# Performance work log

Measured on AMD Instinct MI355X. Metric: run time of the kernel, lower is better.

The kernel has to match this reference:

```python
import jax, jax.numpy as jnp
import numpy as np

N, M, D = 2048, 50000, 128


def setup_inputs() -> dict:
    key = jax.random.key(0)
    kz, kr = jax.random.split(key)
    z = jax.random.normal(kz, (N, D), dtype=jnp.float32)
    ref = jax.random.normal(kr, (M, D), dtype=jnp.float32)  # stands in for the concatenated in_dl batches
    return {"z": z, "ref": ref, "k": 10}


def reference(z, ref, k):
    # L2-normalize rows (matches z / z.norm(dim=1, keepdim=True))
    zn = z / jnp.linalg.norm(z, axis=1, keepdims=True)      # [N, D]
    rn = ref / jnp.linalg.norm(ref, axis=1, keepdims=True)  # [M, D]
    # Pairwise L2 distances via ||a||^2 + ||b||^2 - 2 a.b (same math as the
    # broadcast (rep_batch - rep_z).norm(dim=2), without the O(N*M*D) blowup).
    sq = (jnp.sum(zn * zn, axis=1)[:, None]
          + jnp.sum(rn * rn, axis=1)[None, :]
          - 2.0 * jnp.einsum('nd,md->nm', zn, rn))          # [N, M]
    dist = jnp.sqrt(jnp.maximum(sq, 1e-12))
    # Full sort along the reference axis, take the k-th smallest distance.
    return jnp.sort(dist, axis=1)[:, k]                      # [N]
```

## Files before the change

### kernel.cpp

```cpp
#include <hip/hip_runtime.h>


#define D_DIM 128
#define TQB 256
#define BR 64
#define NCH 64
#define NSUB (NCH * 16)
#define KK 11
#define CAP 256

typedef __bf16 bf16_t;
typedef bf16_t bf16x8 __attribute__((ext_vector_type(8)));
typedef float f32x16 __attribute__((ext_vector_type(16)));

__device__ __forceinline__ unsigned short f2bf(float f) {
    unsigned u = __float_as_uint(f);
    return (unsigned short)((u + 0x7fffu + ((u >> 16) & 1u)) >> 16);
}

__global__ __launch_bounds__(256) void normalize_bf16(
    const float* __restrict__ z, const float* __restrict__ ref,
    unsigned short* __restrict__ zb, unsigned short* __restrict__ rb,
    int N, int M)
{
    const int w = threadIdx.x >> 6;
    const int l = threadIdx.x & 63;
    const int row = blockIdx.x * 4 + w;
    if (row >= N + M) return;
    const float* in; unsigned short* out; int r;
    if (row < N) { in = z;   out = zb; r = row; }
    else         { in = ref; out = rb; r = row - N; }
    const float2 v = ((const float2*)in)[(size_t)r * 64 + l];
    float ss = v.x * v.x + v.y * v.y;
    #pragma unroll
    for (int off = 32; off > 0; off >>= 1) ss += __shfl_xor(ss, off);
    const float inv = rsqrtf(ss);
    ushort2 o; o.x = f2bf(v.x * inv); o.y = f2bf(v.y * inv);
    ((ushort2*)out)[(size_t)r * 64 + l] = o;
}

__device__ __forceinline__ void gld_lds16(const unsigned short* g,
                                          unsigned short* l) {
    __builtin_amdgcn_global_load_lds(
        (__attribute__((address_space(1))) void*)g,
        (__attribute__((address_space(3))) void*)l, 16, 0, 0);
}

template <int PASS>
__global__ __launch_bounds__(512) void knn_pass(
    const unsigned short* __restrict__ zb, const unsigned short* __restrict__ rb,
    float* __restrict__ maxes, const float* __restrict__ T,
    int* __restrict__ cnt, float* __restrict__ surv,
    int N, int M, int chunk)
{
    __shared__ __align__(16) unsigned short Bt[2 * BR * D_DIM];

    const int nwg = 8 * NCH;
    const int bid = (int)blockIdx.x + 8 * (int)blockIdx.y;
    const int swz = (bid & 7) * (nwg >> 3) + (bid >> 3);
    const int bx = swz & 7;
    const int by = swz >> 3;

    const int t = threadIdx.x;
    const int lane = t & 63;
    const int w = t >> 6;
    const int quad = lane >> 4;
    const int ln = lane & 15;
    const int l31 = lane & 31;
    const int hi = lane >> 5;
    const int rbase = bx * TQB + w * 32;
    const int row = rbase + l31;
    const int c0 = by * chunk;
    const int c1 = min(c0 + chunk, M);
    const int clen = c1 - c0;
    const int nt = (clen + BR - 1) / BR;

    bf16x8 qfr[8];
    #pragma unroll
    for (int ks = 0; ks < 8; ++ks)
        qfr[ks] = *(const bf16x8*)
            &zb[(size_t)row * D_DIM + ks * 16 + hi * 8];

    float mx[16];
    float tr = 0.f;
    if (PASS == 1) {
        #pragma unroll
        for (int r = 0; r < 16; ++r) mx[r] = -3.0f;
    } else {
        tr = T[row];
    }

    auto stage = [&](int half, int tile) {
        const int s0 = c0 + tile * BR;
        #pragma unroll
        for (int i = 0; i < 2; ++i) {
            const int r = w * 8 + i * 4 + quad;
            int g = s0 + r; if (g > M - 1) g = M - 1;
            const int sl = ln ^ (r & 15);
            gld_lds16(&rb[(size_t)g * D_DIM + sl * 8],
                      &Bt[half * (BR * D_DIM) + (w * 8 + i * 4) * D_DIM]);
        }
    };

    stage(0, 0);
    stage(1, nt > 1 ? 1 : 0);

    for (int it = 0; it < nt; ++it) {
        if (it + 1 < nt) asm volatile("s_waitcnt vmcnt(2)" ::: "memory");
        else             asm volatile("s_waitcnt vmcnt(0)" ::: "memory");
        __builtin_amdgcn_s_barrier();
        asm volatile("" ::: "memory");
        __builtin_amdgcn_sched_barrier(0);

        const int cur = it & 1;
        const unsigned short* Bc = &Bt[cur * (BR * D_DIM)];

        f32x16 acc0 = {0,0,0,0,0,0,0,0,0,0,0,0,0,0,0,0};
        f32x16 acc1 = {0,0,0,0,0,0,0,0,0,0,0,0,0,0,0,0};

        __builtin_amdgcn_s_setprio(1);
        #pragma unroll
        for (int ks = 0; ks < 8; ++ks) {
            const int sl = ((ks * 2 + hi) ^ ln) * 8;
            bf16x8 a0 = *(const bf16x8*)&Bc[(l31)      * D_DIM + sl];
            bf16x8 a1 = *(const bf16x8*)&Bc[(32 + l31) * D_DIM + sl];
            acc0 = __builtin_amdgcn_mfma_f32_32x32x16_bf16(a0, qfr[ks], acc0, 0, 0, 0);
            acc1 = __builtin_amdgcn_mfma_f32_32x32x16_bf16(a1, qfr[ks], acc1, 0, 0, 0);
        }
        __builtin_amdgcn_s_setprio(0);

        const int rem = clen - it * BR;
        if (rem >= BR) {
            if (PASS == 1) {
                #pragma unroll
                for (int r = 0; r < 16; ++r)
                    mx[r] = fmaxf(mx[r], fmaxf(acc0[r], acc1[r]));
            } else {
                #pragma unroll
                for (int r = 0; r < 16; ++r) {
                    float v0 = acc0[r], v1 = acc1[r];
                    if (v0 >= tr) {
                        int slot = atomicAdd(&cnt[row], 1);
                        if (slot < CAP) surv[(size_t)row * CAP + slot] = v0;
                    }
                    if (v1 >= tr) {
                        int slot = atomicAdd(&cnt[row], 1);
                        if (slot < CAP) surv[(size_t)row * CAP + slot] = v1;
                    }
                }
            }
        } else {
            #pragma unroll
            for (int r = 0; r < 16; ++r) {
                const int crow = (r & 3) + 8 * (r >> 2) + 4 * hi;
                const bool ok0 = crow < rem;
                const bool ok1 = 32 + crow < rem;
                if (PASS == 1) {
                    if (ok0) mx[r] = fmaxf(mx[r], acc0[r]);
                    if (ok1) mx[r] = fmaxf(mx[r], acc1[r]);
                } else {
                    float v0 = acc0[r], v1 = acc1[r];
                    if (ok0 && v0 >= tr) {
                        int slot = atomicAdd(&cnt[row], 1);
                        if (slot < CAP) surv[(size_t)row * CAP + slot] = v0;
                    }
                    if (ok1 && v1 >= tr) {
                        int slot = atomicAdd(&cnt[row], 1);
                        if (slot < CAP) surv[(size_t)row * CAP + slot] = v1;
                    }
                }
            }
        }

        __builtin_amdgcn_sched_barrier(0);
        asm volatile("" ::: "memory");
        __builtin_amdgcn_s_barrier();
        if (it + 2 < nt) stage(cur, it + 2);
    }

    if (PASS == 1) {
        #pragma unroll
        for (int r = 0; r < 16; ++r) {
            float m2 = fmaxf(mx[r], __shfl_xor(mx[r], 32));
            if (hi == 0)
                maxes[(size_t)row * NSUB + by * 16 + r] = m2;
        }
    }
}

__device__ __forceinline__ float kth_largest_64(float* s, int kk, int t) {
    float cur = -3.0f;
    for (int it = 0; it <= kk; ++it) {
        float m = s[0];
        #pragma unroll
        for (int off = 32; off > 0; off >>= 1) m = fmaxf(m, __shfl_xor(m, off));
        cur = m;
        unsigned long long b = __ballot(s[0] == m);
        bool owner = ((int)(__ffsll(b) - 1) == t);
        #pragma unroll
        for (int j = 0; j < KK - 1; ++j) s[j] = owner ? s[j + 1] : s[j];
        if (owner) s[KK - 1] = -3.0f;
    }
    return cur;
}

__global__ __launch_bounds__(64) void knn_threshold(
    const float* __restrict__ maxes, const int* __restrict__ kp,
    float* __restrict__ T, int* __restrict__ cnt)
{
    const int row = blockIdx.x;
    const int t = threadIdx.x;
    float s[KK];
    #pragma unroll
    for (int j = 0; j < KK; ++j) s[j] = -3.0f;
    #pragma unroll
    for (int i = 0; i < NSUB / 64; ++i) {
        float v = maxes[(size_t)row * NSUB + t + 64 * i];
        #pragma unroll
        for (int j = 0; j < KK; ++j) {
            float hi = fmaxf(s[j], v), lo = fminf(s[j], v);
            s[j] = hi; v = lo;
        }
    }
    const int kk = *kp;
    float cur = kth_largest_64(s, kk, t);
    if (t == 0) { T[row] = cur; cnt[row] = 0; }
}

__global__ __launch_bounds__(64) void knn_final(
    const float* __restrict__ surv, const int* __restrict__ cnt,
    const int* __restrict__ kp, float* __restrict__ out)
{
    const int row = blockIdx.x;
    const int t = threadIdx.x;
    int c = cnt[row]; if (c > CAP) c = CAP;
    float s[KK];
    #pragma unroll
    for (int j = 0; j < KK; ++j) s[j] = -3.0f;
    #pragma unroll
    for (int i = 0; i < CAP / 64; ++i) {
        int idx = t + 64 * i;
        float v = (idx < c) ? surv[(size_t)row * CAP + idx] : -3.0f;
        #pragma unroll
        for (int j = 0; j < KK; ++j) {
            float hi = fmaxf(s[j], v), lo = fminf(s[j], v);
            s[j] = hi; v = lo;
        }
    }
    const int kk = *kp;
    float cur = kth_largest_64(s, kk, t);
    if (t == 0) out[row] = sqrtf(fmaxf(2.0f - 2.0f * cur, 1e-12f));
}

extern "C" void kernel_launch(void* const* d_in, const int* in_sizes, int n_in,
                              void* d_out, int out_size, void* d_ws, size_t ws_size,
                              hipStream_t stream) {
    const float* z   = (const float*)d_in[0];
    const float* ref = (const float*)d_in[1];
    const int*   kp  = (const int*)d_in[2];
    float* out = (float*)d_out;

    const int N = in_sizes[0] / D_DIM;
    const int M = in_sizes[1] / D_DIM;

    unsigned short* zbuf = (unsigned short*)d_ws;
    unsigned short* rbuf = zbuf + (size_t)N * D_DIM;
    float* maxes = (float*)(rbuf + (size_t)M * D_DIM);
    float* T     = maxes + (size_t)N * NSUB;
    int*   cnt   = (int*)(T + N);
    float* surv  = (float*)(cnt + N);

    normalize_bf16<<<(N + M + 3) / 4, 256, 0, stream>>>(z, ref, zbuf, rbuf, N, M);

    const int chunk = (M + NCH - 1) / NCH;
    dim3 grid(N / TQB, NCH);

    knn_pass<1><<<grid, 512, 0, stream>>>(zbuf, rbuf, maxes, nullptr,
                                          nullptr, nullptr, N, M, chunk);
    knn_threshold<<<N, 64, 0, stream>>>(maxes, kp, T, cnt);
    knn_pass<2><<<grid, 512, 0, stream>>>(zbuf, rbuf, nullptr, T,
                                          cnt, surv, N, M, chunk);
    knn_final<<<N, 64, 0, stream>>>(surv, cnt, kp, out);
}
```

Measured before the change: 165.3 us.

## Replace second full GEMM pass with targeted rescan of candidate subgroups

The second full distance pass over all reference rows is dropped. The first pass now stores per-lane-half maxima, giving finer subgroups. The threshold kernel picks the subgroups whose max reaches the k-th largest max, and a new per-query rescan kernel recomputes exact dot products only for the members of those subgroups, then selects the k-th. This removes roughly half the MFMA and streaming work, in exchange for scattered per-row dot products and a slow full-scan fallback when there are too many candidates.

```diff
diff --git a/kernel.cpp b/kernel.cpp
--- a/kernel.cpp
+++ b/kernel.cpp
@@ -5,9 +5,11 @@
 #define TQB 256
 #define BR 64
 #define NCH 64
-#define NSUB (NCH * 16)
+#define NSUB (NCH * 32)
 #define KK 11
-#define CAP 256
+#define NCAND 32
+#define SLOTS 26
+#define DN 2816
 
 typedef __bf16 bf16_t;
 typedef bf16_t bf16x8 __attribute__((ext_vector_type(8)));
@@ -46,12 +48,9 @@
         (__attribute__((address_space(3))) void*)l, 16, 0, 0);
 }
 
-template <int PASS>
-__global__ __launch_bounds__(512) void knn_pass(
+__global__ __launch_bounds__(512) void knn_maxes(
     const unsigned short* __restrict__ zb, const unsigned short* __restrict__ rb,
-    float* __restrict__ maxes, const float* __restrict__ T,
-    int* __restrict__ cnt, float* __restrict__ surv,
-    int N, int M, int chunk)
+    float* __restrict__ maxes, int N, int M, int chunk)
 {
     __shared__ __align__(16) unsigned short Bt[2 * BR * D_DIM];
 
@@ -68,8 +67,7 @@
     const int ln = lane & 15;
     const int l31 = lane & 31;
     const int hi = lane >> 5;
-    const int rbase = bx * TQB + w * 32;
-    const int row = rbase + l31;
+    const int row = bx * TQB + w * 32 + l31;
     const int c0 = by * chunk;
     const int c1 = min(c0 + chunk, M);
     const int clen = c1 - c0;
@@ -78,17 +76,11 @@
     bf16x8 qfr[8];
     #pragma unroll
     for (int ks = 0; ks < 8; ++ks)
-        qfr[ks] = *(const bf16x8*)
-            &zb[(size_t)row * D_DIM + ks * 16 + hi * 8];
+        qfr[ks] = *(const bf16x8*)&zb[(size_t)row * D_DIM + ks * 16 + hi * 8];
 
     float mx[16];
-    float tr = 0.f;
-    if (PASS == 1) {
-        #pragma unroll
-        for (int r = 0; r < 16; ++r) mx[r] = -3.0f;
-    } else {
-        tr = T[row];
-    }
+    #pragma unroll
+    for (int r = 0; r < 16; ++r) mx[r] = -3.0f;
 
     auto stage = [&](int half, int tile) {
         const int s0 = c0 + tile * BR;
@@ -131,44 +123,15 @@
 
         const int rem = clen - it * BR;
         if (rem >= BR) {
-            if (PASS == 1) {
-                #pragma unroll
-                for (int r = 0; r < 16; ++r)
-                    mx[r] = fmaxf(mx[r], fmaxf(acc0[r], acc1[r]));
-            } else {
-                #pragma unroll
-                for (int r = 0; r < 16; ++r) {
-                    float v0 = acc0[r], v1 = acc1[r];
-                    if (v0 >= tr) {
-                        int slot = atomicAdd(&cnt[row], 1);
-                        if (slot < CAP) surv[(size_t)row * CAP + slot] = v0;
-                    }
-                    if (v1 >= tr) {
-                        int slot = atomicAdd(&cnt[row], 1);
-                        if (slot < CAP) surv[(size_t)row * CAP + slot] = v1;
-                    }
-                }
-            }
+            #pragma unroll
+            for (int r = 0; r < 16; ++r)
+                mx[r] = fmaxf(mx[r], fmaxf(acc0[r], acc1[r]));
         } else {
             #pragma unroll
             for (int r = 0; r < 16; ++r) {
                 const int crow = (r & 3) + 8 * (r >> 2) + 4 * hi;
-                const bool ok0 = crow < rem;
-                const bool ok1 = 32 + crow < rem;
-                if (PASS == 1) {
-                    if (ok0) mx[r] = fmaxf(mx[r], acc0[r]);
-                    if (ok1) mx[r] = fmaxf(mx[r], acc1[r]);
-                } else {
-                    float v0 = acc0[r], v1 = acc1[r];
-                    if (ok0 && v0 >= tr) {
-                        int slot = atomicAdd(&cnt[row], 1);
-                        if (slot < CAP) surv[(size_t)row * CAP + slot] = v0;
-                    }
-                    if (ok1 && v1 >= tr) {
-                        int slot = atomicAdd(&cnt[row], 1);
-                        if (slot < CAP) surv[(size_t)row * CAP + slot] = v1;
-                    }
-                }
+                if (crow < rem)      mx[r] = fmaxf(mx[r], acc0[r]);
+                if (32 + crow < rem) mx[r] = fmaxf(mx[r], acc1[r]);
             }
         }
 
@@ -178,13 +141,11 @@
         if (it + 2 < nt) stage(cur, it + 2);
     }
 
-    if (PASS == 1) {
-        #pragma unroll
-        for (int r = 0; r < 16; ++r) {
-            float m2 = fmaxf(mx[r], __shfl_xor(mx[r], 32));
-            if (hi == 0)
-                maxes[(size_t)row * NSUB + by * 16 + r] = m2;
-        }
+    float* mp = &maxes[(size_t)row * NSUB + by * 32 + hi * 16];
+    #pragma unroll
+    for (int r4 = 0; r4 < 4; ++r4) {
+        float4 v4 = { mx[r4 * 4], mx[r4 * 4 + 1], mx[r4 * 4 + 2], mx[r4 * 4 + 3] };
+        *(float4*)&mp[r4 * 4] = v4;
     }
 }
 
@@ -206,7 +167,7 @@
 
 __global__ __launch_bounds__(64) void knn_threshold(
     const float* __restrict__ maxes, const int* __restrict__ kp,
-    float* __restrict__ T, int* __restrict__ cnt)
+    int* __restrict__ cand, int* __restrict__ ccnt)
 {
     const int row = blockIdx.x;
     const int t = threadIdx.x;
@@ -223,33 +184,110 @@
         }
     }
     const int kk = *kp;
-    float cur = kth_largest_64(s, kk, t);
-    if (t == 0) { T[row] = cur; cnt[row] = 0; }
-}
-
-__global__ __launch_bounds__(64) void knn_final(
-    const float* __restrict__ surv, const int* __restrict__ cnt,
-    const int* __restrict__ kp, float* __restrict__ out)
+    const float T = kth_largest_64(s, kk, t);
+
+    __shared__ int cn;
+    if (t == 0) cn = 0;
+    __syncthreads();
+    #pragma unroll
+    for (int i = 0; i < NSUB / 64; ++i) {
+        float v = maxes[(size_t)row * NSUB + t + 64 * i];
+        if (v >= T) {
+            int slot = atomicAdd(&cn, 1);
+            if (slot < NCAND) cand[(size_t)row * NCAND + slot] = t + 64 * i;
+        }
+    }
+    __syncthreads();
+    if (t == 0) ccnt[row] = cn;
+}
+
+__global__ __launch_bounds__(256) void knn_rescan(
+    const unsigned short* __restrict__ zb, const unsigned short* __restrict__ rb,
+    const int* __restrict__ cand, const int* __restrict__ ccnt,
+    const int* __restrict__ kp, float* __restrict__ out,
+    int M, int chunk)
 {
     const int row = blockIdx.x;
     const int t = threadIdx.x;
-    int c = cnt[row]; if (c > CAP) c = CAP;
-    float s[KK];
-    #pragma unroll
-    for (int j = 0; j < KK; ++j) s[j] = -3.0f;
-    #pragma unroll
-    for (int i = 0; i < CAP / 64; ++i) {
-        int idx = t + 64 * i;
-        float v = (idx < c) ? surv[(size_t)row * CAP + idx] : -3.0f;
-        #pragma unroll
-        for (int j = 0; j < KK; ++j) {
-            float hi = fmaxf(s[j], v), lo = fminf(s[j], v);
-            s[j] = hi; v = lo;
-        }
-    }
+    __shared__ float qs[D_DIM];
+    __shared__ float dbuf[DN];
+
+    if (t < D_DIM)
+        qs[t] = (float)(((const bf16_t*)zb)[(size_t)row * D_DIM + t]);
+    for (int i = t; i < DN; i += 256) dbuf[i] = -3.0f;
+    __syncthreads();
+
+    const int cn = ccnt[row];
     const int kk = *kp;
-    float cur = kth_largest_64(s, kk, t);
-    if (t == 0) out[row] = sqrtf(fmaxf(2.0f - 2.0f * cur, 1e-12f));
+
+    auto dot_of = [&](int ref) -> float {
+        const unsigned short* rp = &rb[(size_t)ref * D_DIM];
+        float acc = 0.f;
+        #pragma unroll
+        for (int j = 0; j < D_DIM; j += 8) {
+            bf16x8 rv = *(const bf16x8*)(rp + j);
+            const float4 q0 = *(const float4*)&qs[j];
+            const float4 q1 = *(const float4*)&qs[j + 4];
+            acc = fmaf((float)rv[0], q0.x, acc);
+            acc = fmaf((float)rv[1], q0.y, acc);
+            acc = fmaf((float)rv[2], q0.z, acc);
+            acc = fmaf((float)rv[3], q0.w, acc);
+            acc = fmaf((float)rv[4], q1.x, acc);
+            acc = fmaf((float)rv[5], q1.y, acc);
+            acc = fmaf((float)rv[6], q1.z, acc);
+            acc = fmaf((float)rv[7], q1.w, acc);
+        }
+        return acc;
+    };
+
+    if (cn <= NCAND) {
+        const int work = cn * SLOTS;
+        for (int gs = t; gs < work; gs += 256) {
+            const int ci = gs / SLOTS;
+            const int sl = gs - ci * SLOTS;
+            const int s  = cand[(size_t)row * NCAND + ci];
+            const int by = s >> 5;
+            const int r  = s & 15;
+            const int h2 = (s >> 4) & 1;
+            const int base = (r & 3) + 8 * (r >> 2) + 4 * h2;
+            const int c0 = by * chunk;
+            const int c1 = min(c0 + chunk, M);
+            const int ref = c0 + (sl >> 1) * 64 + (sl & 1) * 32 + base;
+            if (ref < c1) dbuf[gs] = dot_of(ref);
+        }
+    } else {
+        float s[KK];
+        #pragma unroll
+        for (int j = 0; j < KK; ++j) s[j] = -3.0f;
+        for (int g = t; g < M; g += 256) {
+            float v = dot_of(g);
+            #pragma unroll
+            for (int j = 0; j < KK; ++j) {
+                float hi = fmaxf(s[j], v), lo = fminf(s[j], v);
+                s[j] = hi; v = lo;
+            }
+        }
+        #pragma unroll
+        for (int j = 0; j < KK; ++j) dbuf[t * KK + j] = s[j];
+    }
+    __syncthreads();
+
+    if (t < 64) {
+        float s[KK];
+        #pragma unroll
+        for (int j = 0; j < KK; ++j) s[j] = -3.0f;
+        #pragma unroll
+        for (int j = 0; j < DN / 64; ++j) {
+            float v = dbuf[t + 64 * j];
+            #pragma unroll
+            for (int q = 0; q < KK; ++q) {
+                float hi = fmaxf(s[q], v), lo = fminf(s[q], v);
+                s[q] = hi; v = lo;
+            }
+        }
+        const float cur = kth_largest_64(s, kk, t);
+        if (t == 0) out[row] = sqrtf(fmaxf(2.0f - 2.0f * cur, 1e-12f));
+    }
 }
 
 extern "C" void kernel_launch(void* const* d_in, const int* in_sizes, int n_in,
@@ -266,19 +304,15 @@
     unsigned short* zbuf = (unsigned short*)d_ws;
     unsigned short* rbuf = zbuf + (size_t)N * D_DIM;
     float* maxes = (float*)(rbuf + (size_t)M * D_DIM);
-    float* T     = maxes + (size_t)N * NSUB;
-    int*   cnt   = (int*)(T + N);
-    float* surv  = (float*)(cnt + N);
+    int*   cand  = (int*)(maxes + (size_t)N * NSUB);
+    int*   ccnt  = cand + (size_t)N * NCAND;
 
     normalize_bf16<<<(N + M + 3) / 4, 256, 0, stream>>>(z, ref, zbuf, rbuf, N, M);
 
     const int chunk = (M + NCH - 1) / NCH;
     dim3 grid(N / TQB, NCH);
 
-    knn_pass<1><<<grid, 512, 0, stream>>>(zbuf, rbuf, maxes, nullptr,
-                                          nullptr, nullptr, N, M, chunk);
-    knn_threshold<<<N, 64, 0, stream>>>(maxes, kp, T, cnt);
-    knn_pass<2><<<grid, 512, 0, stream>>>(zbuf, rbuf, nullptr, T,
-                                          cnt, surv, N, M, chunk);
-    knn_final<<<N, 64, 0, stream>>>(surv, cnt, kp, out);
-}
+    knn_maxes<<<grid, 512, 0, stream>>>(zbuf, rbuf, maxes, N, M, chunk);
+    knn_threshold<<<N, 64, 0, stream>>>(maxes, kp, cand, ccnt);
+    knn_rescan<<<N, 256, 0, stream>>>(zbuf, rbuf, cand, ccnt, kp, out, M, chunk);
+}
```

Result: slower. 174.4 us (+5.5%).
